# Kernel optimization log

Measured on AMD Instinct MI355X. Metric: run time of the kernel, lower is better.

The kernel has to match this reference:

```python
import jax, jax.numpy as jnp
import numpy as np

S_LEN, T_LEN, BATCH, HID = 32, 32, 64, 512


def setup_inputs() -> dict:
    key = jax.random.key(0)
    ks = jax.random.split(key, 5)
    H = HID
    sc = lambda n: 1.0 / np.sqrt(n)
    return {
        "source": jax.random.normal(ks[0], (S_LEN, BATCH, H), jnp.float32),
        "target": jax.random.normal(ks[1], (T_LEN, BATCH, H), jnp.float32),
        # H2h Dense: concat(s_h, t_h) [B, 2H] -> [B, H], linear
        "W_H2h": (jax.random.normal(ks[2], (2 * H, H), jnp.float32) * sc(2 * H)),
        "b_H2h": jnp.zeros((H,), jnp.float32),
        # shared LSTMCell weights (Keras gate order i, f, g, o)
        "W_kernel": (jax.random.normal(ks[3], (H, 4 * H), jnp.float32) * sc(H)),
        "W_rec": (jax.random.normal(ks[4], (H, 4 * H), jnp.float32) * sc(H)),
        "b_lstm": jnp.zeros((4 * H,), jnp.float32),
    }


def _lstm_cell(x, h, c, Wk, Wr, b):
    # Keras LSTMCell math, gate order i, f, g(candidate), o
    z = x @ Wk + h @ Wr + b  # [B, 4H]
    i, f, g, o = jnp.split(z, 4, axis=-1)
    c2 = jax.nn.sigmoid(f) * c + jax.nn.sigmoid(i) * jnp.tanh(g)
    h2 = jax.nn.sigmoid(o) * jnp.tanh(c2)
    return h2, c2


def reference(source, target, W_H2h, b_H2h, W_kernel, W_rec, b_lstm):
    # source: [S, B, H] (time-major), target: [T, B, H]
    T, B, H = target.shape

    def inner(s_state, t_slice):
        # s_state carried along the target axis; t_slice is target cell j state
        s_step, s_h, s_m = s_state
        t_step, t_h, t_m = t_slice
        hmid = jnp.concatenate([s_h, t_h], axis=1) @ W_H2h + b_H2h  # [B, H]
        ns_h, ns_m = _lstm_cell(s_step, hmid, s_m, W_kernel, W_rec, b_lstm)
        nt_h, nt_m = _lstm_cell(t_step, hmid, t_m, W_kernel, W_rec, b_lstm)
        # step arrays get overwritten with the new hidden state
        return (ns_h, ns_h, ns_m), (nt_h, nt_h, nt_m)

    def outer(t_arrays, s_in):
        # fresh source state per outer step i: step = source[i], h = m = 0
        z = jnp.zeros_like(s_in)
        (s_step_f, _, _), t_new = jax.lax.scan(inner, (s_in, z, z), t_arrays)
        return t_new, s_step_f

    zeros = jnp.zeros((T, B, H), source.dtype)
    t_final, source_out = jax.lax.scan(outer, (target, zeros, zeros), source)
    return source_out, t_final[0]
```

## Files before the change

kernel.cpp:

```cpp
#include <hip/hip_runtime.h>

#define BLK 256

typedef __bf16 bf16;
typedef __bf16 bf16x8 __attribute__((ext_vector_type(8)));
typedef float f32x4 __attribute__((ext_vector_type(4)));

__device__ __forceinline__ float sigm(float x) { return 1.f / (1.f + __expf(-x)); }
__device__ __forceinline__ float tanh_(float x) {
    x = fminf(fmaxf(x, -15.f), 15.f);
    float e = __expf(2.f * x);
    return (e - 1.f) / (e + 1.f);
}

__device__ __forceinline__ void gl2lds(const bf16* g, bf16* l) {
    __builtin_amdgcn_global_load_lds((const __attribute__((address_space(1))) void*)g,
                                     (__attribute__((address_space(3))) void*)l, 16, 0, 0);
}

__global__ __launch_bounds__(256) void k_prep(
    const float* __restrict__ src, const float* __restrict__ tgt,
    const float* __restrict__ WH, const float* __restrict__ bH,
    const float* __restrict__ Wk, const float* __restrict__ Wr,
    const float* __restrict__ bl,
    bf16* __restrict__ srcb, bf16* __restrict__ tgtb,
    bf16* __restrict__ WHhi, bf16* __restrict__ WHlo,
    bf16* __restrict__ Wrhi, bf16* __restrict__ Wrlo,
    bf16* __restrict__ P2, float* __restrict__ bz) {
    __shared__ float tile[64][65];
    const int bid = blockIdx.x, t = threadIdx.x;
    if (bid < 512) {
        const float* in = (bid < 256) ? Wr : Wk;
        bf16* ohi = (bid < 256) ? Wrhi : P2;
        bf16* olo = (bid < 256) ? Wrlo : nullptr;
        const int b = bid & 255;
        const int tr = b >> 5, tc = b & 31;
#pragma unroll
        for (int q = 0; q < 16; q++) {
            int idx = q * 256 + t, lr = idx >> 6, lc = idx & 63;
            tile[lr][lc] = in[(size_t)(tr * 64 + lr) * 2048 + tc * 64 + lc];
        }
        __syncthreads();
#pragma unroll
        for (int q = 0; q < 16; q++) {
            int idx = q * 256 + t, lr = idx >> 6, lc = idx & 63;
            float v = tile[lc][lr];
            size_t o = (size_t)(tc * 64 + lr) * 512 + tr * 64 + lc;
            bf16 h = (bf16)v;
            ohi[o] = h;
            if (olo) olo[o] = (bf16)(v - (float)h);
        }
    } else if (bid < 520) {
        int c = (bid - 512) * 256 + t;
        float s = bl[c];
        for (int k = 0; k < 512; k++) s += bH[k] * Wr[(size_t)k * 2048 + c];
        bz[c] = s;
    } else {
        const int gt = (bid - 520) * 256 + t, NT = 504 * 256;
        for (int id = gt; id < 1048576; id += NT) srcb[id] = (bf16)src[id];
        for (int id = gt; id < 1048576; id += NT) tgtb[id] = (bf16)tgt[id];
        for (int id = gt; id < 524288; id += NT) {
            float v = WH[id];
            bf16 h = (bf16)v;
            WHhi[id] = h;
            WHlo[id] = (bf16)(v - (float)h);
        }
    }
}

__global__ __launch_bounds__(256, 4) void k_gemmP(
    const bf16* __restrict__ Wrhi, const bf16* __restrict__ Wrlo,
    const bf16* __restrict__ WHhi, const bf16* __restrict__ WHlo,
    const float* __restrict__ Wk,
    bf16* __restrict__ P1, bf16* __restrict__ P3,
    bf16* __restrict__ P4, bf16* __restrict__ P5) {
    __shared__ __align__(16) bf16 At[64 * 64];
    __shared__ __align__(16) bf16 Bt[128 * 64];
    const int t = threadIdx.x, w = t >> 6, l = t & 63;
    const int m0 = (blockIdx.x >> 3) * 64, n0 = (blockIdx.x & 7) * 128;
    f32x4 acc[2][4] = {};
    const bf16* Aps[3] = {Wrhi, Wrlo, Wrhi};
    const bf16* Bps[3] = {WHhi, WHhi, WHlo};
    for (int ph = 0; ph < 3; ph++) {
        const bf16* Ap = Aps[ph] + (size_t)m0 * 512;
        const bf16* Bp = Bps[ph] + (size_t)n0 * 512;
        for (int kt = 0; kt < 8; kt++) {
            int k0 = kt * 64;
            __syncthreads();
#pragma unroll
            for (int q = 0; q < 2; q++) {
                int pp = q * 256 + t;
                int r = pp >> 3, c = (pp & 7) ^ (r & 7);
                gl2lds(Ap + (size_t)r * 512 + k0 + c * 8, &At[(q * 256 + w * 64) * 8]);
            }
#pragma unroll
            for (int q = 0; q < 4; q++) {
                int pp = q * 256 + t;
                int r = pp >> 3, c = (pp & 7) ^ (r & 7);
                gl2lds(Bp + (size_t)r * 512 + k0 + c * 8, &Bt[(q * 256 + w * 64) * 8]);
            }
            __syncthreads();
#pragma unroll
            for (int ks = 0; ks < 2; ks++) {
                int c = ks * 4 + (l >> 4);
                bf16x8 af[2], bb[4];
#pragma unroll
                for (int mt = 0; mt < 2; mt++) {
                    int r = (w >> 1) * 32 + mt * 16 + (l & 15);
                    af[mt] = *(const bf16x8*)&At[(r * 8 + (c ^ (r & 7))) * 8];
                }
#pragma unroll
                for (int g = 0; g < 4; g++) {
                    int r = g * 32 + (w & 1) * 16 + (l & 15);
                    bb[g] = *(const bf16x8*)&Bt[(r * 8 + (c ^ (r & 7))) * 8];
                }
#pragma unroll
                for (int mt = 0; mt < 2; mt++)
#pragma unroll
                    for (int g = 0; g < 4; g++)
                        acc[mt][g] = __builtin_amdgcn_mfma_f32_16x16x32_bf16(
                            af[mt], bb[g], acc[mt][g], 0, 0, 0);
            }
        }
    }
    const bool hihalf = (n0 >= 512);
#pragma unroll
    for (int mt = 0; mt < 2; mt++) {
#pragma unroll
        for (int g = 0; g < 4; g++) {
            int np = n0 + g * 32 + (w & 1) * 16 + (l & 15);
#pragma unroll
            for (int r = 0; r < 4; r++) {
                int c = m0 + (w >> 1) * 32 + mt * 16 + ((l >> 4) << 2) + r;
                float v = acc[mt][g][r];
                if (!hihalf) {
                    P4[(size_t)c * 512 + np] = (bf16)v;
                    P1[(size_t)c * 512 + np] = (bf16)(v + Wk[(size_t)np * 2048 + c]);
                } else {
                    int kk = np - 512;
                    P3[(size_t)c * 512 + kk] = (bf16)v;
                    P5[(size_t)c * 512 + kk] = (bf16)(v + Wk[(size_t)kk * 2048 + c]);
                }
            }
        }
    }
}

__global__ __launch_bounds__(256, 4) void k_diag6(
    int d, int i_lo,
    const bf16* __restrict__ srcb, const bf16* __restrict__ tgtb,
    const bf16* __restrict__ P1, const bf16* __restrict__ P2,
    const bf16* __restrict__ P3, const bf16* __restrict__ P4,
    const bf16* __restrict__ P5,
    const float* __restrict__ bz,
    const bf16* __restrict__ shR, bf16* __restrict__ shW,
    const bf16* __restrict__ thR, bf16* __restrict__ thW,
    float* __restrict__ sc, float* __restrict__ tc,
    float* __restrict__ out) {
    __shared__ __align__(16) bf16 At[64 * 64];
    __shared__ __align__(16) bf16 Bt[128 * 64];
    const int t = threadIdx.x, w = t >> 6, l = t & 63;
    const int cell = blockIdx.x >> 5, sub = blockIdx.x & 31;
    const int side = sub >> 4, ch0 = (sub & 15) << 5;
    const int i = i_lo + cell, j = d - i;
    const size_t stI = (size_t)i * 32768, stJ = (size_t)j * 32768;

    const bf16* Ah[2];
    const bf16* Wh[2];
    int nh = 0;
    if (side == 0) {
        Ah[nh] = (j == 0 ? srcb : shR) + stI;
        Wh[nh] = (j == 0 ? P2 : P1);
        nh++;
        if (i > 0) { Ah[nh] = thR + stJ; Wh[nh] = P3; nh++; }
    } else {
        if (j > 0) { Ah[nh] = shR + stI; Wh[nh] = P4; nh++; }
        Ah[nh] = (i == 0 ? tgtb : thR) + stJ;
        Wh[nh] = (i == 0 ? P2 : P5);
        nh++;
    }

    f32x4 acc[2][4] = {};
    for (int hh = 0; hh < nh; hh++) {
        const bf16* Ap = Ah[hh];
        const bf16* Wp = Wh[hh];
#pragma unroll 1
        for (int kt = 0; kt < 8; kt++) {
            int k0 = kt * 64;
            __syncthreads();
#pragma unroll
            for (int q = 0; q < 2; q++) {
                int pp = q * 256 + t;
                int r = pp >> 3, c = (pp & 7) ^ (r & 7);
                gl2lds(Ap + (size_t)r * 512 + k0 + c * 8, &At[(q * 256 + w * 64) * 8]);
            }
#pragma unroll
            for (int q = 0; q < 4; q++) {
                int pp = q * 256 + t;
                int r = pp >> 3, c = (pp & 7) ^ (r & 7);
                size_t grow = (size_t)((r >> 5) * 512 + ch0 + (r & 31));
                gl2lds(Wp + grow * 512 + k0 + c * 8, &Bt[(q * 256 + w * 64) * 8]);
            }
            __syncthreads();
#pragma unroll
            for (int ks = 0; ks < 2; ks++) {
                int cq = ks * 4 + (l >> 4);
                bf16x8 af[2], bb[4];
#pragma unroll
                for (int mt = 0; mt < 2; mt++) {
                    int r = (w >> 1) * 32 + mt * 16 + (l & 15);
                    af[mt] = *(const bf16x8*)&At[(r * 8 + (cq ^ (r & 7))) * 8];
                }
#pragma unroll
                for (int g = 0; g < 4; g++) {
                    int r = g * 32 + (w & 1) * 16 + (l & 15);
                    bb[g] = *(const bf16x8*)&Bt[(r * 8 + (cq ^ (r & 7))) * 8];
                }
#pragma unroll
                for (int mt = 0; mt < 2; mt++)
#pragma unroll
                    for (int g = 0; g < 4; g++)
                        acc[mt][g] = __builtin_amdgcn_mfma_f32_16x16x32_bf16(
                            af[mt], bb[g], acc[mt][g], 0, 0, 0);
            }
        }
    }

    const int h = ch0 + (w & 1) * 16 + (l & 15);
    float bzv[4];
#pragma unroll
    for (int g = 0; g < 4; g++) bzv[g] = bz[g * 512 + h];
#pragma unroll
    for (int mt = 0; mt < 2; mt++) {
#pragma unroll
        for (int r = 0; r < 4; r++) {
            int b = (w >> 1) * 32 + mt * 16 + ((l >> 4) << 2) + r;
            float zi = acc[mt][0][r] + bzv[0];
            float zf = acc[mt][1][r] + bzv[1];
            float zg = acc[mt][2][r] + bzv[2];
            float zo = acc[mt][3][r] + bzv[3];
            if (side == 0) {
                size_t off = stI + (size_t)b * 512 + h;
                float cold = (j == 0) ? 0.f : sc[off];
                float c2 = sigm(zf) * cold + sigm(zi) * tanh_(zg);
                float h2 = sigm(zo) * tanh_(c2);
                sc[off] = c2;
                shW[off] = (bf16)h2;
                if (j == 31) out[off] = h2;
            } else {
                size_t off = stJ + (size_t)b * 512 + h;
                float cold = (i == 0) ? 0.f : tc[off];
                float c2 = sigm(zf) * cold + sigm(zi) * tanh_(zg);
                float h2 = sigm(zo) * tanh_(c2);
                tc[off] = c2;
                thW[off] = (bf16)h2;
                if (i == 31) out[1048576 + off] = h2;
            }
        }
    }
}


extern "C" void kernel_launch(void* const* d_in, const int* in_sizes, int n_in,
                              void* d_out, int out_size, void* d_ws, size_t ws_size,
                              hipStream_t stream) {
    char* w = (char*)d_ws;
    const size_t MB = 1u << 20;
    const float* src = (const float*)d_in[0];
    const float* tgt = (const float*)d_in[1];
    const float* WH = (const float*)d_in[2];
    const float* bH = (const float*)d_in[3];
    const float* Wk = (const float*)d_in[4];
    const float* Wr = (const float*)d_in[5];
    const float* bl = (const float*)d_in[6];
    float* out = (float*)d_out;

    bf16* srcb = (bf16*)(w + 0 * MB);
    bf16* tgtb = (bf16*)(w + 2 * MB);
    bf16* WHhi = (bf16*)(w + 4 * MB);
    bf16* WHlo = (bf16*)(w + 5 * MB);
    bf16* Wrhi = (bf16*)(w + 6 * MB);
    bf16* Wrlo = (bf16*)(w + 8 * MB);
    bf16* P1 = (bf16*)(w + 10 * MB);
    bf16* P2 = (bf16*)(w + 12 * MB);
    bf16* P3 = (bf16*)(w + 14 * MB);
    bf16* P4 = (bf16*)(w + 16 * MB);
    bf16* P5 = (bf16*)(w + 18 * MB);
    float* bz = (float*)(w + 20 * MB);
    bf16* sh = (bf16*)(w + 21 * MB);
    bf16* th = (bf16*)(w + 25 * MB);
    float* sc = (float*)(w + 29 * MB);
    float* tc = (float*)(w + 33 * MB);

    k_prep<<<1024, BLK, 0, stream>>>(src, tgt, WH, bH, Wk, Wr, bl, srcb, tgtb,
                                     WHhi, WHlo, Wrhi, Wrlo, P2, bz);
    k_gemmP<<<256, BLK, 0, stream>>>(Wrhi, Wrlo, WHhi, WHlo, Wk, P1, P3, P4, P5);

    for (int d = 0; d < 63; d++) {
        int i_lo = d > 31 ? d - 31 : 0;
        int i_hi = d < 31 ? d : 31;
        int Kd = i_hi - i_lo + 1;
        const bf16* shR = sh + (size_t)(d & 1) * 1048576;
        bf16* shW = sh + (size_t)((d + 1) & 1) * 1048576;
        const bf16* thR = th + (size_t)(d & 1) * 1048576;
        bf16* thW = th + (size_t)((d + 1) & 1) * 1048576;
        k_diag6<<<Kd * 32, BLK, 0, stream>>>(d, i_lo, srcb, tgtb, P1, P2, P3, P4, P5,
                                             bz, shR, shW, thR, thW, sc, tc, out);
    }
}
```

Before: 1.425 ms.

## Double-buffer LDS tiles in diagonal LSTM kernel to overlap loads with MFMA

The diagonal kernel's K loop now uses two LDS buffers for the A and B tiles. The next tile is issued with global_load_lds while MFMAs run on the current one, so each iteration needs one wait and barrier instead of two syncthreads. The loop over both matrix halves is flattened into a single pipelined loop. LDS use per block doubles, and the launch-bounds occupancy hint drops from 4 to 3 blocks per CU.

```diff
diff --git a/kernel.cpp b/kernel.cpp
--- a/kernel.cpp
+++ b/kernel.cpp
@@ -146,7 +146,7 @@
     }
 }
 
-__global__ __launch_bounds__(256, 4) void k_diag6(
+__global__ __launch_bounds__(256, 3) void k_diag8(
     int d, int i_lo,
     const bf16* __restrict__ srcb, const bf16* __restrict__ tgtb,
     const bf16* __restrict__ P1, const bf16* __restrict__ P2,
@@ -157,8 +157,8 @@
     const bf16* __restrict__ thR, bf16* __restrict__ thW,
     float* __restrict__ sc, float* __restrict__ tc,
     float* __restrict__ out) {
-    __shared__ __align__(16) bf16 At[64 * 64];
-    __shared__ __align__(16) bf16 Bt[128 * 64];
+    __shared__ __align__(16) bf16 At[2][64 * 64];
+    __shared__ __align__(16) bf16 Bt[2][128 * 64];
     const int t = threadIdx.x, w = t >> 6, l = t & 63;
     const int cell = blockIdx.x >> 5, sub = blockIdx.x & 31;
     const int side = sub >> 4, ch0 = (sub & 15) << 5;
@@ -181,49 +181,66 @@
     }
 
     f32x4 acc[2][4] = {};
-    for (int hh = 0; hh < nh; hh++) {
-        const bf16* Ap = Ah[hh];
-        const bf16* Wp = Wh[hh];
+    const int R = nh * 8;
+
+    auto STAGE = [&](int bf, int rr) {
+        const bf16* Ap = Ah[rr >> 3];
+        const bf16* Wp = Wh[rr >> 3];
+        const int k0 = (rr & 7) * 64;
+        bf16* A = &At[bf][0];
+        bf16* B = &Bt[bf][0];
+#pragma unroll
+        for (int q = 0; q < 2; q++) {
+            int pp = q * 256 + t;
+            int rA = pp >> 3, cA = (pp & 7) ^ (rA & 7);
+            gl2lds(Ap + (size_t)rA * 512 + k0 + cA * 8, &A[(q * 256 + w * 64) * 8]);
+        }
+#pragma unroll
+        for (int q = 0; q < 4; q++) {
+            int pp = q * 256 + t;
+            int rB = pp >> 3, cB = (pp & 7) ^ (rB & 7);
+            size_t grow = (size_t)((rB >> 5) * 512 + ch0 + (rB & 31));
+            gl2lds(Wp + grow * 512 + k0 + cB * 8, &B[(q * 256 + w * 64) * 8]);
+        }
+    };
+
+    auto COMPUTE = [&](int bf) {
+        const bf16* A = &At[bf][0];
+        const bf16* B = &Bt[bf][0];
+#pragma unroll
+        for (int ks = 0; ks < 2; ks++) {
+            int cq = ks * 4 + (l >> 4);
+            bf16x8 af[2], bb[4];
+#pragma unroll
+            for (int mt = 0; mt < 2; mt++) {
+                int rr = (w >> 1) * 32 + mt * 16 + (l & 15);
+                af[mt] = *(const bf16x8*)&A[(rr * 8 + (cq ^ (rr & 7))) * 8];
+            }
+#pragma unroll
+            for (int g = 0; g < 4; g++) {
+                int rr = g * 32 + (w & 1) * 16 + (l & 15);
+                bb[g] = *(const bf16x8*)&B[(rr * 8 + (cq ^ (rr & 7))) * 8];
+            }
+#pragma unroll
+            for (int mt = 0; mt < 2; mt++)
+#pragma unroll
+                for (int g = 0; g < 4; g++)
+                    acc[mt][g] = __builtin_amdgcn_mfma_f32_16x16x32_bf16(
+                        af[mt], bb[g], acc[mt][g], 0, 0, 0);
+        }
+    };
+
+    STAGE(0, 0);
+    asm volatile("s_waitcnt vmcnt(0)" ::: "memory");
+    __builtin_amdgcn_s_barrier();
+    int bf = 0;
 #pragma unroll 1
-        for (int kt = 0; kt < 8; kt++) {
-            int k0 = kt * 64;
-            __syncthreads();
-#pragma unroll
-            for (int q = 0; q < 2; q++) {
-                int pp = q * 256 + t;
-                int r = pp >> 3, c = (pp & 7) ^ (r & 7);
-                gl2lds(Ap + (size_t)r * 512 + k0 + c * 8, &At[(q * 256 + w * 64) * 8]);
-            }
-#pragma unroll
-            for (int q = 0; q < 4; q++) {
-                int pp = q * 256 + t;
-                int r = pp >> 3, c = (pp & 7) ^ (r & 7);
-                size_t grow = (size_t)((r >> 5) * 512 + ch0 + (r & 31));
-                gl2lds(Wp + grow * 512 + k0 + c * 8, &Bt[(q * 256 + w * 64) * 8]);
-            }
-            __syncthreads();
-#pragma unroll
-            for (int ks = 0; ks < 2; ks++) {
-                int cq = ks * 4 + (l >> 4);
-                bf16x8 af[2], bb[4];
-#pragma unroll
-                for (int mt = 0; mt < 2; mt++) {
-                    int r = (w >> 1) * 32 + mt * 16 + (l & 15);
-                    af[mt] = *(const bf16x8*)&At[(r * 8 + (cq ^ (r & 7))) * 8];
-                }
-#pragma unroll
-                for (int g = 0; g < 4; g++) {
-                    int r = g * 32 + (w & 1) * 16 + (l & 15);
-                    bb[g] = *(const bf16x8*)&Bt[(r * 8 + (cq ^ (r & 7))) * 8];
-                }
-#pragma unroll
-                for (int mt = 0; mt < 2; mt++)
-#pragma unroll
-                    for (int g = 0; g < 4; g++)
-                        acc[mt][g] = __builtin_amdgcn_mfma_f32_16x16x32_bf16(
-                            af[mt], bb[g], acc[mt][g], 0, 0, 0);
-            }
-        }
+    for (int rr = 0; rr < R; rr++) {
+        if (rr + 1 < R) STAGE(bf ^ 1, rr + 1);
+        COMPUTE(bf);
+        asm volatile("s_waitcnt vmcnt(0)" ::: "memory");
+        __builtin_amdgcn_s_barrier();
+        bf ^= 1;
     }
 
     const int h = ch0 + (w & 1) * 16 + (l & 15);
@@ -304,7 +321,7 @@
         bf16* shW = sh + (size_t)((d + 1) & 1) * 1048576;
         const bf16* thR = th + (size_t)(d & 1) * 1048576;
         bf16* thW = th + (size_t)((d + 1) & 1) * 1048576;
-        k_diag6<<<Kd * 32, BLK, 0, stream>>>(d, i_lo, srcb, tgtb, P1, P2, P3, P4, P5,
+        k_diag8<<<Kd * 32, BLK, 0, stream>>>(d, i_lo, srcb, tgtb, P1, P2, P3, P4, P5,
                                              bz, shR, shW, thR, thW, sc, tc, out);
     }
 }
```

Result: slower. 2.400 ms (+68.5%).

## Replace per-diagonal kernel launches with one persistent cooperative kernel using grid sync

Applied to the files above, without the earlier changes.

Folds the 63 per-anti-diagonal launches into a single cooperative kernel. The kernel loops over diagonals, spreads work items over a grid sized to the occupancy limit, and uses grid.sync between diagonals. It also doubles the K tile to 128, with a larger LDS footprint and 16-way swizzle, and drops the blocks-per-CU hint from 4 to 3. This removes launch overhead and gaps between launches, at the cost of grid-wide barrier latency, fewer resident blocks, and grid-stride imbalance on wide diagonals of up to 1024 items.

```diff
diff --git a/kernel.cpp b/kernel.cpp
--- a/kernel.cpp
+++ b/kernel.cpp
@@ -1,6 +1,9 @@
 #include <hip/hip_runtime.h>
+#include <hip/hip_cooperative_groups.h>
 
 #define BLK 256
+
+namespace cg = cooperative_groups;
 
 typedef __bf16 bf16;
 typedef __bf16 bf16x8 __attribute__((ext_vector_type(8)));
@@ -146,117 +149,135 @@
     }
 }
 
-__global__ __launch_bounds__(256, 4) void k_diag6(
-    int d, int i_lo,
+__global__ __launch_bounds__(256, 3) void k_coop(
     const bf16* __restrict__ srcb, const bf16* __restrict__ tgtb,
     const bf16* __restrict__ P1, const bf16* __restrict__ P2,
     const bf16* __restrict__ P3, const bf16* __restrict__ P4,
     const bf16* __restrict__ P5,
     const float* __restrict__ bz,
-    const bf16* __restrict__ shR, bf16* __restrict__ shW,
-    const bf16* __restrict__ thR, bf16* __restrict__ thW,
+    bf16* __restrict__ sh, bf16* __restrict__ th,
     float* __restrict__ sc, float* __restrict__ tc,
     float* __restrict__ out) {
-    __shared__ __align__(16) bf16 At[64 * 64];
-    __shared__ __align__(16) bf16 Bt[128 * 64];
+    __shared__ __align__(16) bf16 At[64 * 128];
+    __shared__ __align__(16) bf16 Bt[128 * 128];
     const int t = threadIdx.x, w = t >> 6, l = t & 63;
-    const int cell = blockIdx.x >> 5, sub = blockIdx.x & 31;
-    const int side = sub >> 4, ch0 = (sub & 15) << 5;
-    const int i = i_lo + cell, j = d - i;
-    const size_t stI = (size_t)i * 32768, stJ = (size_t)j * 32768;
-
-    const bf16* Ah[2];
-    const bf16* Wh[2];
-    int nh = 0;
-    if (side == 0) {
-        Ah[nh] = (j == 0 ? srcb : shR) + stI;
-        Wh[nh] = (j == 0 ? P2 : P1);
-        nh++;
-        if (i > 0) { Ah[nh] = thR + stJ; Wh[nh] = P3; nh++; }
-    } else {
-        if (j > 0) { Ah[nh] = shR + stI; Wh[nh] = P4; nh++; }
-        Ah[nh] = (i == 0 ? tgtb : thR) + stJ;
-        Wh[nh] = (i == 0 ? P2 : P5);
-        nh++;
-    }
-
-    f32x4 acc[2][4] = {};
-    for (int hh = 0; hh < nh; hh++) {
-        const bf16* Ap = Ah[hh];
-        const bf16* Wp = Wh[hh];
+    cg::grid_group grid = cg::this_grid();
+    const int G = gridDim.x;
+
+    for (int d = 0; d < 63; d++) {
+        const int i_lo = d > 31 ? d - 31 : 0;
+        const int i_hi = d < 31 ? d : 31;
+        const int Kd = i_hi - i_lo + 1;
+        const bf16* shR = sh + (size_t)(d & 1) * 1048576;
+        bf16* shW = sh + (size_t)((d + 1) & 1) * 1048576;
+        const bf16* thR = th + (size_t)(d & 1) * 1048576;
+        bf16* thW = th + (size_t)((d + 1) & 1) * 1048576;
+
+        for (int item = blockIdx.x; item < Kd * 32; item += G) {
+            const int cell = item >> 5, sub = item & 31;
+            const int side = sub >> 4, ch0 = (sub & 15) << 5;
+            const int i = i_lo + cell, j = d - i;
+            const size_t stI = (size_t)i * 32768, stJ = (size_t)j * 32768;
+
+            const bf16* Ah[2];
+            const bf16* Wh[2];
+            int nh = 0;
+            if (side == 0) {
+                Ah[nh] = (j == 0 ? srcb : shR) + stI;
+                Wh[nh] = (j == 0 ? P2 : P1);
+                nh++;
+                if (i > 0) { Ah[nh] = thR + stJ; Wh[nh] = P3; nh++; }
+            } else {
+                if (j > 0) { Ah[nh] = shR + stI; Wh[nh] = P4; nh++; }
+                Ah[nh] = (i == 0 ? tgtb : thR) + stJ;
+                Wh[nh] = (i == 0 ? P2 : P5);
+                nh++;
+            }
+
+            f32x4 acc[2][4] = {};
+            for (int hh = 0; hh < nh; hh++) {
+                const bf16* Ap = Ah[hh];
+                const bf16* Wp = Wh[hh];
 #pragma unroll 1
-        for (int kt = 0; kt < 8; kt++) {
-            int k0 = kt * 64;
-            __syncthreads();
-#pragma unroll
-            for (int q = 0; q < 2; q++) {
-                int pp = q * 256 + t;
-                int r = pp >> 3, c = (pp & 7) ^ (r & 7);
-                gl2lds(Ap + (size_t)r * 512 + k0 + c * 8, &At[(q * 256 + w * 64) * 8]);
-            }
-#pragma unroll
-            for (int q = 0; q < 4; q++) {
-                int pp = q * 256 + t;
-                int r = pp >> 3, c = (pp & 7) ^ (r & 7);
-                size_t grow = (size_t)((r >> 5) * 512 + ch0 + (r & 31));
-                gl2lds(Wp + grow * 512 + k0 + c * 8, &Bt[(q * 256 + w * 64) * 8]);
-            }
-            __syncthreads();
-#pragma unroll
-            for (int ks = 0; ks < 2; ks++) {
-                int cq = ks * 4 + (l >> 4);
-                bf16x8 af[2], bb[4];
-#pragma unroll
-                for (int mt = 0; mt < 2; mt++) {
-                    int r = (w >> 1) * 32 + mt * 16 + (l & 15);
-                    af[mt] = *(const bf16x8*)&At[(r * 8 + (cq ^ (r & 7))) * 8];
-                }
-#pragma unroll
-                for (int g = 0; g < 4; g++) {
-                    int r = g * 32 + (w & 1) * 16 + (l & 15);
-                    bb[g] = *(const bf16x8*)&Bt[(r * 8 + (cq ^ (r & 7))) * 8];
-                }
-#pragma unroll
-                for (int mt = 0; mt < 2; mt++)
-#pragma unroll
-                    for (int g = 0; g < 4; g++)
-                        acc[mt][g] = __builtin_amdgcn_mfma_f32_16x16x32_bf16(
-                            af[mt], bb[g], acc[mt][g], 0, 0, 0);
-            }
-        }
-    }
-
-    const int h = ch0 + (w & 1) * 16 + (l & 15);
-    float bzv[4];
-#pragma unroll
-    for (int g = 0; g < 4; g++) bzv[g] = bz[g * 512 + h];
-#pragma unroll
-    for (int mt = 0; mt < 2; mt++) {
-#pragma unroll
-        for (int r = 0; r < 4; r++) {
-            int b = (w >> 1) * 32 + mt * 16 + ((l >> 4) << 2) + r;
-            float zi = acc[mt][0][r] + bzv[0];
-            float zf = acc[mt][1][r] + bzv[1];
-            float zg = acc[mt][2][r] + bzv[2];
-            float zo = acc[mt][3][r] + bzv[3];
-            if (side == 0) {
-                size_t off = stI + (size_t)b * 512 + h;
-                float cold = (j == 0) ? 0.f : sc[off];
-                float c2 = sigm(zf) * cold + sigm(zi) * tanh_(zg);
-                float h2 = sigm(zo) * tanh_(c2);
-                sc[off] = c2;
-                shW[off] = (bf16)h2;
-                if (j == 31) out[off] = h2;
-            } else {
-                size_t off = stJ + (size_t)b * 512 + h;
-                float cold = (i == 0) ? 0.f : tc[off];
-                float c2 = sigm(zf) * cold + sigm(zi) * tanh_(zg);
-                float h2 = sigm(zo) * tanh_(c2);
-                tc[off] = c2;
-                thW[off] = (bf16)h2;
-                if (i == 31) out[1048576 + off] = h2;
-            }
-        }
+                for (int kt = 0; kt < 4; kt++) {
+                    int k0 = kt * 128;
+                    __syncthreads();
+#pragma unroll
+                    for (int q = 0; q < 4; q++) {
+                        int pp = q * 256 + t;
+                        int r = pp >> 4, c = (pp & 15) ^ (r & 15);
+                        gl2lds(Ap + (size_t)r * 512 + k0 + c * 8,
+                               &At[(q * 256 + w * 64) * 8]);
+                    }
+#pragma unroll
+                    for (int q = 0; q < 8; q++) {
+                        int pp = q * 256 + t;
+                        int r = pp >> 4, c = (pp & 15) ^ (r & 15);
+                        int g = r >> 5;
+                        gl2lds(Wp + (size_t)(g * 512 + ch0 + (r & 31)) * 512 + k0 + c * 8,
+                               &Bt[(q * 256 + w * 64) * 8]);
+                    }
+                    __syncthreads();
+#pragma unroll
+                    for (int ks = 0; ks < 4; ks++) {
+                        int cq = ks * 4 + (l >> 4);
+                        bf16x8 af[2], bb[4];
+#pragma unroll
+                        for (int mt = 0; mt < 2; mt++) {
+                            int r = (w >> 1) * 32 + mt * 16 + (l & 15);
+                            af[mt] = *(const bf16x8*)&At[(r * 16 + (cq ^ (r & 15))) * 8];
+                        }
+#pragma unroll
+                        for (int g = 0; g < 4; g++) {
+                            int r = g * 32 + (w & 1) * 16 + (l & 15);
+                            bb[g] = *(const bf16x8*)&Bt[(r * 16 + (cq ^ (r & 15))) * 8];
+                        }
+#pragma unroll
+                        for (int mt = 0; mt < 2; mt++)
+#pragma unroll
+                            for (int g = 0; g < 4; g++)
+                                acc[mt][g] = __builtin_amdgcn_mfma_f32_16x16x32_bf16(
+                                    af[mt], bb[g], acc[mt][g], 0, 0, 0);
+                    }
+                }
+            }
+
+            const int h = ch0 + (w & 1) * 16 + (l & 15);
+            float bzv[4];
+#pragma unroll
+            for (int g = 0; g < 4; g++) bzv[g] = bz[g * 512 + h];
+#pragma unroll
+            for (int mt = 0; mt < 2; mt++) {
+#pragma unroll
+                for (int r = 0; r < 4; r++) {
+                    int b = (w >> 1) * 32 + mt * 16 + ((l >> 4) << 2) + r;
+                    float zi = acc[mt][0][r] + bzv[0];
+                    float zf = acc[mt][1][r] + bzv[1];
+                    float zg = acc[mt][2][r] + bzv[2];
+                    float zo = acc[mt][3][r] + bzv[3];
+                    if (side == 0) {
+                        size_t off = stI + (size_t)b * 512 + h;
+                        float cold = (j == 0) ? 0.f : sc[off];
+                        float c2 = sigm(zf) * cold + sigm(zi) * tanh_(zg);
+                        float h2 = sigm(zo) * tanh_(c2);
+                        sc[off] = c2;
+                        shW[off] = (bf16)h2;
+                        if (j == 31) out[off] = h2;
+                    } else {
+                        size_t off = stJ + (size_t)b * 512 + h;
+                        float cold = (i == 0) ? 0.f : tc[off];
+                        float c2 = sigm(zf) * cold + sigm(zi) * tanh_(zg);
+                        float h2 = sigm(zo) * tanh_(c2);
+                        tc[off] = c2;
+                        thW[off] = (bf16)h2;
+                        if (i == 31) out[1048576 + off] = h2;
+                    }
+                }
+            }
+        }
+
+        asm volatile("s_waitcnt vmcnt(0)" ::: "memory");
+        grid.sync();
     }
 }
 
@@ -292,19 +313,27 @@
     float* sc = (float*)(w + 29 * MB);
     float* tc = (float*)(w + 33 * MB);
 
+    static int G = 0;
+    if (G == 0) {
+        int dev = 0;
+        hipGetDevice(&dev);
+        hipDeviceProp_t prop;
+        int nCU = 256;
+        if (hipGetDeviceProperties(&prop, dev) == hipSuccess && prop.multiProcessorCount > 0)
+            nCU = prop.multiProcessorCount;
+        int nb = 0;
+        if (hipOccupancyMaxActiveBlocksPerMultiprocessor(&nb, k_coop, BLK, 0) != hipSuccess ||
+            nb < 1)
+            nb = 3;
+        if (nb > 3) nb = 3;
+        G = nb * nCU;
+    }
+
     k_prep<<<1024, BLK, 0, stream>>>(src, tgt, WH, bH, Wk, Wr, bl, srcb, tgtb,
                                      WHhi, WHlo, Wrhi, Wrlo, P2, bz);
     k_gemmP<<<256, BLK, 0, stream>>>(Wrhi, Wrlo, WHhi, WHlo, Wk, P1, P3, P4, P5);
 
-    for (int d = 0; d < 63; d++) {
-        int i_lo = d > 31 ? d - 31 : 0;
-        int i_hi = d < 31 ? d : 31;
-        int Kd = i_hi - i_lo + 1;
-        const bf16* shR = sh + (size_t)(d & 1) * 1048576;
-        bf16* shW = sh + (size_t)((d + 1) & 1) * 1048576;
-        const bf16* thR = th + (size_t)(d & 1) * 1048576;
-        bf16* thW = th + (size_t)((d + 1) & 1) * 1048576;
-        k_diag6<<<Kd * 32, BLK, 0, stream>>>(d, i_lo, srcb, tgtb, P1, P2, P3, P4, P5,
-                                             bz, shR, shW, thR, thW, sc, tc, out);
-    }
-}
+    void* args[] = {&srcb, &tgtb, &P1, &P2, &P3, &P4, &P5,
+                    &bz, &sh, &th, &sc, &tc, &out};
+    hipLaunchCooperativeKernel((void*)k_coop, dim3(G), dim3(BLK), args, 0, stream);
+}
```

Result: slower. 3.925 ms (+175.4%).

## Pair two diagonal cells per block to reuse weight tiles across 128 rows

Applied to the files above, without the earlier changes.

Each block now processes two wavefront cells (128 batch rows) against the same 128-gate weight tile, so every weight tile loaded into LDS serves twice as many MFMAs. This halves the number of blocks and the total weight traffic per diagonal. Edge cells that need different weight matrices (i==0 or j==0) are kept unpaired by a special pairing scheme for d<=31. The cost is a larger LDS A tile and more accumulators, with occupancy lowered to 3 blocks, and fewer blocks on short diagonals.

```diff
diff --git a/kernel.cpp b/kernel.cpp
--- a/kernel.cpp
+++ b/kernel.cpp
@@ -146,8 +146,8 @@
     }
 }
 
-__global__ __launch_bounds__(256, 4) void k_diag6(
-    int d, int i_lo,
+__global__ __launch_bounds__(256, 3) void k_diag9(
+    int d, int i_lo, int Kd,
     const bf16* __restrict__ srcb, const bf16* __restrict__ tgtb,
     const bf16* __restrict__ P1, const bf16* __restrict__ P2,
     const bf16* __restrict__ P3, const bf16* __restrict__ P4,
@@ -157,42 +157,65 @@
     const bf16* __restrict__ thR, bf16* __restrict__ thW,
     float* __restrict__ sc, float* __restrict__ tc,
     float* __restrict__ out) {
-    __shared__ __align__(16) bf16 At[64 * 64];
+    __shared__ __align__(16) bf16 At[128 * 64];
     __shared__ __align__(16) bf16 Bt[128 * 64];
     const int t = threadIdx.x, w = t >> 6, l = t & 63;
-    const int cell = blockIdx.x >> 5, sub = blockIdx.x & 31;
+    const int p = blockIdx.x >> 5, sub = blockIdx.x & 31;
     const int side = sub >> 4, ch0 = (sub & 15) << 5;
-    const int i = i_lo + cell, j = d - i;
-    const size_t stI = (size_t)i * 32768, stJ = (size_t)j * 32768;
-
-    const bf16* Ah[2];
-    const bf16* Wh[2];
+
+    int c0, c1;
+    if (d <= 31) {
+        if (p == 0) { c0 = c1 = 0; }
+        else if (2 * p - 1 <= d - 1) {
+            c0 = 2 * p - 1;
+            c1 = (2 * p <= d - 1) ? 2 * p : c0;
+        } else { c0 = c1 = d; }
+    } else {
+        c0 = 2 * p;
+        c1 = (c0 + 1 < Kd) ? c0 + 1 : c0;
+    }
+    const bool dup = (c0 == c1);
+    const int i0 = i_lo + c0, j0 = d - i0;
+    const int i1 = i_lo + c1, j1 = d - i1;
+    const size_t stI0 = (size_t)i0 * 32768, stJ0 = (size_t)j0 * 32768;
+    const size_t stI1 = (size_t)i1 * 32768, stJ1 = (size_t)j1 * 32768;
+
+    const bf16 *A0h[2], *A1h[2], *Wh[2];
     int nh = 0;
     if (side == 0) {
-        Ah[nh] = (j == 0 ? srcb : shR) + stI;
-        Wh[nh] = (j == 0 ? P2 : P1);
+        A0h[nh] = (j0 == 0 ? srcb : shR) + stI0;
+        A1h[nh] = (j1 == 0 ? srcb : shR) + stI1;
+        Wh[nh] = (j0 == 0 ? P2 : P1);
         nh++;
-        if (i > 0) { Ah[nh] = thR + stJ; Wh[nh] = P3; nh++; }
+        if (i0 > 0) {
+            A0h[nh] = thR + stJ0; A1h[nh] = thR + stJ1; Wh[nh] = P3; nh++;
+        }
     } else {
-        if (j > 0) { Ah[nh] = shR + stI; Wh[nh] = P4; nh++; }
-        Ah[nh] = (i == 0 ? tgtb : thR) + stJ;
-        Wh[nh] = (i == 0 ? P2 : P5);
+        if (j0 > 0) {
+            A0h[nh] = shR + stI0; A1h[nh] = shR + stI1; Wh[nh] = P4; nh++;
+        }
+        A0h[nh] = (i0 == 0 ? tgtb : thR) + stJ0;
+        A1h[nh] = (i1 == 0 ? tgtb : thR) + stJ1;
+        Wh[nh] = (i0 == 0 ? P2 : P5);
         nh++;
     }
 
-    f32x4 acc[2][4] = {};
+    f32x4 acc[4][4] = {};
     for (int hh = 0; hh < nh; hh++) {
-        const bf16* Ap = Ah[hh];
+        const bf16* A0 = A0h[hh];
+        const bf16* A1 = A1h[hh];
         const bf16* Wp = Wh[hh];
 #pragma unroll 1
         for (int kt = 0; kt < 8; kt++) {
-            int k0 = kt * 64;
+            const int k0 = kt * 64;
             __syncthreads();
 #pragma unroll
-            for (int q = 0; q < 2; q++) {
+            for (int q = 0; q < 4; q++) {
                 int pp = q * 256 + t;
                 int r = pp >> 3, c = (pp & 7) ^ (r & 7);
-                gl2lds(Ap + (size_t)r * 512 + k0 + c * 8, &At[(q * 256 + w * 64) * 8]);
+                const bf16* s = (r < 64) ? (A0 + (size_t)r * 512)
+                                         : (A1 + (size_t)(r - 64) * 512);
+                gl2lds(s + k0 + c * 8, &At[(q * 256 + w * 64) * 8]);
             }
 #pragma unroll
             for (int q = 0; q < 4; q++) {
@@ -205,11 +228,11 @@
 #pragma unroll
             for (int ks = 0; ks < 2; ks++) {
                 int cq = ks * 4 + (l >> 4);
-                bf16x8 af[2], bb[4];
-#pragma unroll
-                for (int mt = 0; mt < 2; mt++) {
-                    int r = (w >> 1) * 32 + mt * 16 + (l & 15);
-                    af[mt] = *(const bf16x8*)&At[(r * 8 + (cq ^ (r & 7))) * 8];
+                bf16x8 af[4], bb[4];
+#pragma unroll
+                for (int mm = 0; mm < 4; mm++) {
+                    int r = (mm >> 1) * 64 + (w >> 1) * 32 + (mm & 1) * 16 + (l & 15);
+                    af[mm] = *(const bf16x8*)&At[(r * 8 + (cq ^ (r & 7))) * 8];
                 }
 #pragma unroll
                 for (int g = 0; g < 4; g++) {
@@ -217,11 +240,11 @@
                     bb[g] = *(const bf16x8*)&Bt[(r * 8 + (cq ^ (r & 7))) * 8];
                 }
 #pragma unroll
-                for (int mt = 0; mt < 2; mt++)
+                for (int mm = 0; mm < 4; mm++)
 #pragma unroll
                     for (int g = 0; g < 4; g++)
-                        acc[mt][g] = __builtin_amdgcn_mfma_f32_16x16x32_bf16(
-                            af[mt], bb[g], acc[mt][g], 0, 0, 0);
+                        acc[mm][g] = __builtin_amdgcn_mfma_f32_16x16x32_bf16(
+                            af[mm], bb[g], acc[mm][g], 0, 0, 0);
             }
         }
     }
@@ -231,30 +254,34 @@
 #pragma unroll
     for (int g = 0; g < 4; g++) bzv[g] = bz[g * 512 + h];
 #pragma unroll
-    for (int mt = 0; mt < 2; mt++) {
+    for (int mm = 0; mm < 4; mm++) {
+        const int half = mm >> 1;
+        if (dup && half) continue;
+        const int ii = half ? i1 : i0, jj = half ? j1 : j0;
+        const size_t sI = half ? stI1 : stI0, sJ = half ? stJ1 : stJ0;
 #pragma unroll
         for (int r = 0; r < 4; r++) {
-            int b = (w >> 1) * 32 + mt * 16 + ((l >> 4) << 2) + r;
-            float zi = acc[mt][0][r] + bzv[0];
-            float zf = acc[mt][1][r] + bzv[1];
-            float zg = acc[mt][2][r] + bzv[2];
-            float zo = acc[mt][3][r] + bzv[3];
+            int b = (w >> 1) * 32 + (mm & 1) * 16 + ((l >> 4) << 2) + r;
+            float zi = acc[mm][0][r] + bzv[0];
+            float zf = acc[mm][1][r] + bzv[1];
+            float zg = acc[mm][2][r] + bzv[2];
+            float zo = acc[mm][3][r] + bzv[3];
             if (side == 0) {
-                size_t off = stI + (size_t)b * 512 + h;
-                float cold = (j == 0) ? 0.f : sc[off];
+                size_t off = sI + (size_t)b * 512 + h;
+                float cold = (jj == 0) ? 0.f : sc[off];
                 float c2 = sigm(zf) * cold + sigm(zi) * tanh_(zg);
                 float h2 = sigm(zo) * tanh_(c2);
                 sc[off] = c2;
                 shW[off] = (bf16)h2;
-                if (j == 31) out[off] = h2;
+                if (jj == 31) out[off] = h2;
             } else {
-                size_t off = stJ + (size_t)b * 512 + h;
-                float cold = (i == 0) ? 0.f : tc[off];
+                size_t off = sJ + (size_t)b * 512 + h;
+                float cold = (ii == 0) ? 0.f : tc[off];
                 float c2 = sigm(zf) * cold + sigm(zi) * tanh_(zg);
                 float h2 = sigm(zo) * tanh_(c2);
                 tc[off] = c2;
                 thW[off] = (bf16)h2;
-                if (i == 31) out[1048576 + off] = h2;
+                if (ii == 31) out[1048576 + off] = h2;
             }
         }
     }
@@ -300,11 +327,13 @@
         int i_lo = d > 31 ? d - 31 : 0;
         int i_hi = d < 31 ? d : 31;
         int Kd = i_hi - i_lo + 1;
+        int nPairs = (d <= 31) ? (d == 0 ? 1 : d / 2 + 2) : ((Kd + 1) >> 1);
         const bf16* shR = sh + (size_t)(d & 1) * 1048576;
         bf16* shW = sh + (size_t)((d + 1) & 1) * 1048576;
         const bf16* thR = th + (size_t)(d & 1) * 1048576;
         bf16* thW = th + (size_t)((d + 1) & 1) * 1048576;
-        k_diag6<<<Kd * 32, BLK, 0, stream>>>(d, i_lo, srcb, tgtb, P1, P2, P3, P4, P5,
-                                             bz, shR, shW, thR, thW, sc, tc, out);
-    }
-}
+        k_diag9<<<nPairs * 32, BLK, 0, stream>>>(d, i_lo, Kd, srcb, tgtb,
+                                                 P1, P2, P3, P4, P5, bz,
+                                                 shR, shW, thR, thW, sc, tc, out);
+    }
+}
```

Measured after the change: 1.743 ms. 1.22x slower.
